# Kernel tuning notes

Measured on AMD Instinct MI355X. Metric: run time of the kernel, lower is better.

## Reference

```python
import jax, jax.numpy as jnp
import numpy as np

S = 10        # spiking_segment_count
TEMP = 50.0

def setup_inputs() -> dict:
    key = jax.random.key(0)
    ks = jax.random.split(key, 6)
    bs, din, dout = 2048, 1024, 1024
    x = jax.random.normal(ks[0], (bs, din), dtype=jnp.float32)
    t = jax.random.uniform(ks[1], (bs,), dtype=jnp.float32)  # in [0,1) subset of [-1,1]
    scale = 1.0 / np.sqrt(din)
    param_W = jax.random.normal(ks[2], (din, dout * S * 3), dtype=jnp.float32) * scale
    param_b = jax.random.normal(ks[3], (dout * S * 3,), dtype=jnp.float32) * 0.01
    norm_W = jax.random.normal(ks[4], (din, dout), dtype=jnp.float32) * scale
    norm_b = jax.random.normal(ks[5], (dout,), dtype=jnp.float32) * 0.01
    return {"x": x, "t": t, "param_W": param_W, "param_b": param_b,
            "norm_W": norm_W, "norm_b": norm_b}

def reference(x, t, param_W, param_b, norm_W, norm_b):
    bs = x.shape[0]
    dout = norm_W.shape[1]
    # param GEMM -> (bs, S, dout, 3)
    params = (x @ param_W + param_b).reshape(bs, S, dout, 3)
    weights = jax.nn.softmax(params[..., 0], axis=1)                 # (bs, S, dout)
    keypoints = jnp.concatenate(
        [jnp.zeros_like(weights[:, :1]), jnp.cumsum(weights, axis=1)], axis=1
    ) * 2.0 - 1.0                                                    # (bs, S+1, dout)
    slopes = jnp.tanh(params[..., 1])
    intercepts = params[..., 2]
    tt = t.reshape(-1, 1, 1)                                         # (bs, 1, 1)
    starts = keypoints[:, :S]
    ends = keypoints[:, 1:]
    residual = slopes * tt + intercepts                              # (bs, S, dout)
    validity = ((tt >= starts) & (tt < ends)) | ((tt == 1.0) & (ends == 1.0))
    vf = validity.astype(x.dtype)
    left_margin = jnp.sum((tt - starts) * vf, axis=1)                # (bs, dout)
    right_margin = jnp.sum((ends - tt) * vf, axis=1)
    lw = jax.nn.sigmoid(-TEMP * left_margin)
    rw = jax.nn.sigmoid(-TEMP * right_margin)
    lv = jnp.concatenate([vf[:, :1], vf[:, :-1]], axis=1)
    rv = jnp.concatenate([vf[:, 1:], vf[:, -1:]], axis=1)
    sw = -(lw + rw - 1.0)
    result = (lw * jnp.sum(residual * lv, axis=1)
              + sw * jnp.sum(residual * vf, axis=1)
              + rw * jnp.sum(residual * rv, axis=1))
    # norm == 'constant': subtract segment-wise integral, add norm_net(x)
    integral = jnp.sum(0.5 * slopes * (ends * ends - starts * starts)
                       + intercepts * weights, axis=1) * 0.5
    norm_target = x @ norm_W + norm_b
    return result - integral + norm_target
```

## Files before the change

kernel.cpp:

```cpp
#include <hip/hip_runtime.h>
#include <cstdint>
#include <cstddef>

#define BS    2048
#define DIN   1024
#define DOUT  1024
#define SSEG  10
#define NPAR  30720
#define NPK   20480
#define NCOL2 21504
#define NLG   10240
#define NT_LG 80
#define NT_SM 168
#define MT    16
#define TAU   5e-5f
#define WL_CAP 1048576u

typedef _Float16 half_t;
typedef __attribute__((ext_vector_type(8))) _Float16 half8;
typedef __attribute__((ext_vector_type(4))) _Float16 half4;
typedef __attribute__((ext_vector_type(2))) _Float16 half2v;
typedef __attribute__((ext_vector_type(4))) float   floatx4;

__device__ __forceinline__ void gload16(const void* g, void* l) {
  __builtin_amdgcn_global_load_lds(
      (const __attribute__((address_space(1))) void*)g,
      (__attribute__((address_space(3))) void*)l, 16, 0, 0);
}

__global__ void k_zero(unsigned* c) { if (threadIdx.x == 0) *c = 0; }

__global__ __launch_bounds__(256) void k_prep(const float* __restrict__ x,
                                              half_t* __restrict__ xh,
                                              half_t* __restrict__ xl,
                                              const float* __restrict__ nW,
                                              half_t* __restrict__ wsm,
                                              unsigned* __restrict__ cnt) {
  int bid = blockIdx.x;
  if (bid < 2048) {
    if (bid == 0 && threadIdx.x == 0) *cnt = 0;
    int i = bid * 256 + threadIdx.x;
    floatx4 v = ((const floatx4*)x)[i];
    half4 h, l;
    #pragma unroll
    for (int c = 0; c < 4; c++) { h[c] = (half_t)v[c]; l[c] = (half_t)(v[c] - (float)h[c]); }
    ((half4*)xh)[i] = h;
    ((half4*)xl)[i] = l;
  } else {
    __shared__ float tile[32][33];
    int b2 = bid - 2048;
    int col0 = (b2 & 31) * 32;
    int k0   = (b2 >> 5) * 32;
    int tx = threadIdx.x & 31;
    int ty = threadIdx.x >> 5;
    #pragma unroll
    for (int r = ty; r < 32; r += 8)
      tile[r][tx] = nW[(size_t)(k0 + r) * DOUT + col0 + tx];
    __syncthreads();
    #pragma unroll
    for (int r = ty; r < 32; r += 8)
      wsm[(size_t)(col0 + r + NPK) * DIN + k0 + tx] = (half_t)tile[tx][r];
  }
}

__global__ __launch_bounds__(256) void k_transw(const float* __restrict__ src,
                                                half_t* __restrict__ wsm,
                                                half_t* __restrict__ wh,
                                                half_t* __restrict__ wlo,
                                                float* __restrict__ wlt) {
  __shared__ float tile[32][384];
  int bx = blockIdx.x;
  int k0 = blockIdx.y * 32;
  int tid = threadIdx.x;
  int s  = bx >> 3;
  int d0 = (bx & 7) * 128;
  const float* sb = src + (size_t)k0 * NPAR + bx * 384;
  for (int i = tid; i < 32 * 96; i += 256) {
    int r = i / 96, q = i - r * 96;
    ((floatx4*)&tile[r][0])[q] = ((const floatx4*)(sb + (size_t)r * NPAR))[q];
  }
  __syncthreads();
  int j   = tid & 127;
  int ks  = (tid >> 7) * 16;
  {
    size_t row = (size_t)(s * 1024 + d0 + j) * DIN + k0 + ks;
    #pragma unroll
    for (int m = 0; m < 16; m++) {
      float raw = tile[ks + m][3 * j];
      float v = raw * 32.0f;
      half_t h = (half_t)v;
      wlt[row + m] = raw;
      wh [row + m] = h;
      wlo[row + m] = (half_t)(v - (float)h);
    }
  }
  #pragma unroll
  for (int c = 0; c < 2; c++) {
    size_t row = (size_t)(s * 2048 + 2 * (d0 + j) + c) * DIN + k0 + ks;
    #pragma unroll
    for (int m = 0; m < 16; m++)
      wsm[row + m] = (half_t)tile[ks + m][3 * j + 1 + c];
  }
}

__device__ __forceinline__ void swizzle_mn(int bid, int* mt, int* nt) {
  int x = bid & 7;
  int g = bid >> 3;
  *mt = g & 15;
  *nt = (g >> 4) * 8 + x;
}

__global__ __launch_bounds__(256) void k_gemm_logit(const half_t* __restrict__ Ah,
                                                    const half_t* __restrict__ Al,
                                                    const half_t* __restrict__ Bh,
                                                    const half_t* __restrict__ Bl,
                                                    float* __restrict__ Lg,
                                                    const float* __restrict__ pb) {
  __shared__ __attribute__((aligned(16))) half_t sAh[128 * 32];
  __shared__ __attribute__((aligned(16))) half_t sAl[128 * 32];
  __shared__ __attribute__((aligned(16))) half_t sBh[128 * 32];
  __shared__ __attribute__((aligned(16))) half_t sBl[128 * 32];
  const int K = DIN;
  int mt, nt;
  swizzle_mn(blockIdx.x, &mt, &nt);
  int m0 = mt * 128, n0 = nt * 128;
  int tid = threadIdx.x, w = tid >> 6, L = tid & 63;
  int wm = (w >> 1) * 64, wn = (w & 1) * 64;
  int l15 = L & 15, quad = L >> 4;

  size_t arow = (size_t)(m0 + w * 16 + (L >> 2)) * K + (L & 3) * 8;
  size_t brow = (size_t)(n0 + w * 16 + (L >> 2)) * K + (L & 3) * 8;
  char* lah = (char*)sAh + w * 1024;
  char* lal = (char*)sAl + w * 1024;
  char* lbh = (char*)sBh + w * 1024;
  char* lbl = (char*)sBl + w * 1024;

  floatx4 acc[4][4] = {};

  for (int k0 = 0; k0 < K; k0 += 32) {
    __syncthreads();
    gload16(Ah + arow + k0,          lah);
    gload16(Ah + arow + 64 * K + k0, lah + 4096);
    gload16(Al + arow + k0,          lal);
    gload16(Al + arow + 64 * K + k0, lal + 4096);
    gload16(Bh + brow + k0,          lbh);
    gload16(Bh + brow + 64 * K + k0, lbh + 4096);
    gload16(Bl + brow + k0,          lbl);
    gload16(Bl + brow + 64 * K + k0, lbl + 4096);
    __syncthreads();

    #pragma unroll
    for (int mi = 0; mi < 4; mi++) {
      half8 afh = *(const half8*)((const char*)sAh + (wm + mi * 16 + l15) * 64 + quad * 16);
      half8 afl = *(const half8*)((const char*)sAl + (wm + mi * 16 + l15) * 64 + quad * 16);
      #pragma unroll
      for (int ni = 0; ni < 4; ni++) {
        half8 bfh = *(const half8*)((const char*)sBh + (wn + ni * 16 + l15) * 64 + quad * 16);
        half8 bfl = *(const half8*)((const char*)sBl + (wn + ni * 16 + l15) * 64 + quad * 16);
        floatx4 a = acc[mi][ni];
        a = __builtin_amdgcn_mfma_f32_16x16x32_f16(afh, bfh, a, 0, 0, 0);
        a = __builtin_amdgcn_mfma_f32_16x16x32_f16(afl, bfh, a, 0, 0, 0);
        a = __builtin_amdgcn_mfma_f32_16x16x32_f16(afh, bfl, a, 0, 0, 0);
        acc[mi][ni] = a;
      }
    }
  }

  #pragma unroll
  for (int ni = 0; ni < 4; ni++) {
    int col = n0 + wn + ni * 16 + l15;
    float bias = pb[(col >> 10) * 3072 + (col & 1023) * 3];
    #pragma unroll
    for (int mi = 0; mi < 4; mi++) {
      int row = m0 + wm + mi * 16 + quad * 4;
      floatx4 v = acc[mi][ni];
      #pragma unroll
      for (int r = 0; r < 4; r++)
        Lg[(size_t)(row + r) * NLG + col] = v[r] * 0.03125f + bias;
    }
  }
}

__global__ __launch_bounds__(256) void k_gemm_sm(const half_t* __restrict__ A,
                                                 const half_t* __restrict__ B,
                                                 half_t* __restrict__ P,
                                                 const float* __restrict__ pb,
                                                 const float* __restrict__ nb) {
  __shared__ __attribute__((aligned(16))) half_t As[128 * 32];
  __shared__ __attribute__((aligned(16))) half_t Bs[128 * 32];
  const int K = DIN;
  int mt, nt;
  swizzle_mn(blockIdx.x, &mt, &nt);
  int m0 = mt * 128, n0 = nt * 128;
  int tid = threadIdx.x, w = tid >> 6, L = tid & 63;
  int wm = (w >> 1) * 64, wn = (w & 1) * 64;
  int l15 = L & 15, quad = L >> 4;

  const half_t* ga = A + (size_t)(m0 + w * 16 + (L >> 2)) * K + (L & 3) * 8;
  const half_t* gb = B + (size_t)(n0 + w * 16 + (L >> 2)) * K + (L & 3) * 8;
  char* lA = (char*)As + w * 1024;
  char* lB = (char*)Bs + w * 1024;

  floatx4 acc[4][4] = {};

  for (int k0 = 0; k0 < K; k0 += 32) {
    __syncthreads();
    gload16(ga + k0,          lA);
    gload16(ga + 64 * K + k0, lA + 4096);
    gload16(gb + k0,          lB);
    gload16(gb + 64 * K + k0, lB + 4096);
    __syncthreads();

    half8 af[4], bf[4];
    #pragma unroll
    for (int mi = 0; mi < 4; mi++)
      af[mi] = *(const half8*)((const char*)As + (wm + mi * 16 + l15) * 64 + quad * 16);
    #pragma unroll
    for (int ni = 0; ni < 4; ni++)
      bf[ni] = *(const half8*)((const char*)Bs + (wn + ni * 16 + l15) * 64 + quad * 16);
    #pragma unroll
    for (int mi = 0; mi < 4; mi++)
      #pragma unroll
      for (int ni = 0; ni < 4; ni++)
        acc[mi][ni] = __builtin_amdgcn_mfma_f32_16x16x32_f16(af[mi], bf[ni], acc[mi][ni], 0, 0, 0);
  }

  #pragma unroll
  for (int ni = 0; ni < 4; ni++) {
    int col = n0 + wn + ni * 16 + l15;
    float bias;
    if (col < NPK) {
      int s = col >> 11, rem = col & 2047;
      bias = pb[s * 3072 + 3 * (rem >> 1) + 1 + (rem & 1)];
    } else {
      bias = nb[col - NPK];
    }
    #pragma unroll
    for (int mi = 0; mi < 4; mi++) {
      int row = m0 + wm + mi * 16 + quad * 4;
      floatx4 v = acc[mi][ni];
      #pragma unroll
      for (int r = 0; r < 4; r++)
        P[(size_t)(row + r) * NCOL2 + col] = (half_t)(v[r] + bias);
    }
  }
}

__device__ __forceinline__ float spiking_eval(const float* p, float tt, float* mind) {
  float mx = -1e30f;
  #pragma unroll
  for (int s = 0; s < SSEG; s++) mx = fmaxf(mx, p[3 * s]);
  float ew[10], wsum = 0.0f;
  #pragma unroll
  for (int s = 0; s < SSEG; s++) { ew[s] = __expf(p[3 * s] - mx); wsum += ew[s]; }
  float inv = 1.0f / wsum;

  float kp[11];
  kp[0] = -1.0f;
  float cum = 0.0f, md = 1e30f;
  #pragma unroll
  for (int s = 0; s < SSEG; s++) {
    cum += ew[s] * inv;
    kp[s + 1] = cum * 2.0f - 1.0f;
    md = fminf(md, fabsf(tt - kp[s + 1]));
  }
  *mind = md;

  float vf[10], resid[10];
  float lm = 0.0f, rm = 0.0f, integ = 0.0f;
  #pragma unroll
  for (int s = 0; s < SSEG; s++) {
    float p1 = p[3 * s + 1], p2 = p[3 * s + 2];
    float e2 = __expf(2.0f * fabsf(p1));
    float th = copysignf(1.0f - 2.0f / (e2 + 1.0f), p1);
    resid[s] = th * tt + p2;
    float st = kp[s], en = kp[s + 1];
    bool v = ((tt >= st) && (tt < en)) || ((tt == 1.0f) && (en == 1.0f));
    float vv = v ? 1.0f : 0.0f;
    vf[s] = vv;
    lm += (tt - st) * vv;
    rm += (en - tt) * vv;
    integ += 0.5f * th * (en * en - st * st) + p2 * (ew[s] * inv);
  }
  float resLV = 0.0f, resV = 0.0f, resRV = 0.0f;
  #pragma unroll
  for (int s = 0; s < SSEG; s++) {
    float lv = (s == 0) ? vf[0] : vf[s - 1];
    float rv = (s == 9) ? vf[9] : vf[s + 1];
    resLV += resid[s] * lv;
    resV  += resid[s] * vf[s];
    resRV += resid[s] * rv;
  }
  float lw = 1.0f / (1.0f + __expf(50.0f * lm));
  float rw = 1.0f / (1.0f + __expf(50.0f * rm));
  float swt = 1.0f - lw - rw;
  return lw * resLV + swt * resV + rw * resRV - 0.5f * integ + p[30];
}

__global__ __launch_bounds__(256) void k_pointwise(const half_t* __restrict__ P,
                                                   const float* __restrict__ Lg,
                                                   const float* __restrict__ t,
                                                   float* __restrict__ out,
                                                   unsigned* __restrict__ cnt,
                                                   unsigned* __restrict__ wl,
                                                   unsigned cap) {
  __shared__ __attribute__((aligned(16))) half_t sp[SSEG * 512];
  int b = blockIdx.x, dg = blockIdx.y, tid = threadIdx.x;
  const half_t* Pb = P + (size_t)b * NCOL2;
  for (int i = tid; i < SSEG * 64; i += 256) {
    int s = i >> 6, e = i & 63;
    ((uint4*)sp)[(s << 6) + e] = ((const uint4*)(Pb + s * 2048 + dg * 512))[e];
  }
  float tt = t[b];
  float nt = (float)Pb[NPK + dg * 256 + tid];
  const float* Lb = Lg + (size_t)b * NLG + dg * 256 + tid;
  __syncthreads();

  float p[31];
  #pragma unroll
  for (int s = 0; s < SSEG; s++) {
    p[3 * s] = Lb[s * 1024];
    half2v hv = ((const half2v*)sp)[s * 256 + tid];
    p[3 * s + 1] = (float)hv.x;
    p[3 * s + 2] = (float)hv.y;
  }
  p[30] = nt;
  float mind;
  float r = spiking_eval(p, tt, &mind);
  int d = dg * 256 + tid;
  out[(size_t)b * DOUT + d] = r;
  if (wl != nullptr && mind < TAU) {
    unsigned idx = atomicAdd(cnt, 1u);
    if (idx < cap) wl[idx] = ((unsigned)b << 10) | (unsigned)d;
  }
}

__global__ __launch_bounds__(256) void k_naive(const float* __restrict__ x,
                                               const float* __restrict__ t,
                                               const float* __restrict__ pW,
                                               const float* __restrict__ pb,
                                               const float* __restrict__ nW,
                                               const float* __restrict__ nb,
                                               float* __restrict__ out,
                                               unsigned* __restrict__ cnt,
                                               unsigned* __restrict__ wl,
                                               unsigned cap) {
  __shared__ float xs[DIN];
  int b = blockIdx.x, dg = blockIdx.y, tid = threadIdx.x;
  for (int i = tid; i < DIN; i += 256) xs[i] = x[(size_t)b * DIN + i];
  __syncthreads();
  int d = dg * 256 + tid;
  float acc[31];
  #pragma unroll
  for (int i = 0; i < 31; i++) acc[i] = 0.0f;
  for (int k = 0; k < DIN; k++) {
    float xv = xs[k];
    const float* wr = pW + (size_t)k * NPAR + 3 * d;
    #pragma unroll
    for (int s = 0; s < SSEG; s++) {
      acc[3 * s]     += xv * wr[s * 3072];
      acc[3 * s + 1] += xv * wr[s * 3072 + 1];
      acc[3 * s + 2] += xv * wr[s * 3072 + 2];
    }
    acc[30] += xv * nW[(size_t)k * DOUT + d];
  }
  #pragma unroll
  for (int s = 0; s < SSEG; s++) {
    acc[3 * s]     += pb[s * 3072 + 3 * d];
    acc[3 * s + 1] += pb[s * 3072 + 3 * d + 1];
    acc[3 * s + 2] += pb[s * 3072 + 3 * d + 2];
  }
  acc[30] += nb[d];
  float mind;
  float r = spiking_eval(acc, t[b], &mind);
  out[(size_t)b * DOUT + d] = r;
  if (wl != nullptr && mind < TAU) {
    unsigned idx = atomicAdd(cnt, 1u);
    if (idx < cap) wl[idx] = ((unsigned)b << 10) | (unsigned)d;
  }
}

__global__ __launch_bounds__(256) void k_redo(const float* __restrict__ x,
                                              const float* __restrict__ t,
                                              const float* __restrict__ pW,
                                              const float* __restrict__ pb,
                                              const float* __restrict__ nW,
                                              const float* __restrict__ nb,
                                              const half_t* __restrict__ P,
                                              const float* __restrict__ WLt,
                                              int haveP,
                                              const unsigned* __restrict__ cnt,
                                              const unsigned* __restrict__ wl,
                                              unsigned cap,
                                              float* __restrict__ out) {
  unsigned n = *cnt;
  if (n > cap) n = cap;
  int lane = threadIdx.x & 63;
  unsigned wave = (blockIdx.x * 256 + threadIdx.x) >> 6;
  unsigned nwaves = (gridDim.x * 256) >> 6;

  for (unsigned e = wave; e < n; e += nwaves) {
    unsigned code = wl[e];
    int b = (int)(code >> 10), d = (int)(code & 1023);

    double lg[10], sl[10], ic[10], nt = 0.0;
    #pragma unroll
    for (int s = 0; s < SSEG; s++) { lg[s] = 0.0; sl[s] = 0.0; ic[s] = 0.0; }

    if (haveP) {
      for (int k = lane; k < DIN; k += 64) {
        double xv = (double)x[(size_t)b * DIN + k];
        #pragma unroll
        for (int s = 0; s < SSEG; s++)
          lg[s] += xv * (double)WLt[(size_t)(s * 1024 + d) * DIN + k];
      }
    } else {
      for (int k = lane; k < DIN; k += 64) {
        double xv = (double)x[(size_t)b * DIN + k];
        const float* wr = pW + (size_t)k * NPAR + 3 * d;
        #pragma unroll
        for (int s = 0; s < SSEG; s++) {
          lg[s] += xv * (double)wr[s * 3072];
          sl[s] += xv * (double)wr[s * 3072 + 1];
          ic[s] += xv * (double)wr[s * 3072 + 2];
        }
        nt += xv * (double)nW[(size_t)k * DOUT + d];
      }
    }
    #pragma unroll
    for (int off = 32; off > 0; off >>= 1) {
      #pragma unroll
      for (int s = 0; s < SSEG; s++) lg[s] += __shfl_down(lg[s], off);
      if (!haveP) {
        #pragma unroll
        for (int s = 0; s < SSEG; s++) {
          sl[s] += __shfl_down(sl[s], off);
          ic[s] += __shfl_down(ic[s], off);
        }
        nt += __shfl_down(nt, off);
      }
    }

    if (lane == 0) {
      double slope[10], icpt[10], ntv;
      if (haveP) {
        const half_t* Pr = P + (size_t)b * NCOL2;
        #pragma unroll
        for (int s = 0; s < SSEG; s++) {
          slope[s] = tanh((double)(float)Pr[s * 2048 + 2 * d]);
          icpt[s]  = (double)(float)Pr[s * 2048 + 2 * d + 1];
        }
        ntv = (double)(float)Pr[NPK + d];
      } else {
        #pragma unroll
        for (int s = 0; s < SSEG; s++) {
          slope[s] = tanh(sl[s] + (double)pb[s * 3072 + 3 * d + 1]);
          icpt[s]  = ic[s] + (double)pb[s * 3072 + 3 * d + 2];
        }
        ntv = nt + (double)nb[d];
      }
      #pragma unroll
      for (int s = 0; s < SSEG; s++) lg[s] += (double)pb[s * 3072 + 3 * d];

      double mx = -1e300;
      #pragma unroll
      for (int s = 0; s < SSEG; s++) mx = fmax(mx, lg[s]);
      double ew[10], ws = 0.0;
      #pragma unroll
      for (int s = 0; s < SSEG; s++) { ew[s] = exp(lg[s] - mx); ws += ew[s]; }

      double kp[11];
      kp[0] = -1.0;
      double cum = 0.0;
      #pragma unroll
      for (int s = 0; s < SSEG; s++) { cum += ew[s] / ws; kp[s + 1] = cum * 2.0 - 1.0; }

      double tt = (double)t[b];
      double vf[10], resid[10], lm = 0.0, rm = 0.0, integ = 0.0;
      #pragma unroll
      for (int s = 0; s < SSEG; s++) {
        double st = kp[s], en = kp[s + 1];
        bool v = ((tt >= st) && (tt < en)) || ((tt == 1.0) && (en == 1.0));
        double vv = v ? 1.0 : 0.0;
        vf[s] = vv;
        resid[s] = slope[s] * tt + icpt[s];
        lm += (tt - st) * vv;
        rm += (en - tt) * vv;
        integ += 0.5 * slope[s] * (en * en - st * st) + icpt[s] * (ew[s] / ws);
      }
      double rLV = 0.0, rV = 0.0, rRV = 0.0;
      #pragma unroll
      for (int s = 0; s < SSEG; s++) {
        double lv = (s == 0) ? vf[0] : vf[s - 1];
        double rv = (s == 9) ? vf[9] : vf[s + 1];
        rLV += resid[s] * lv;
        rV  += resid[s] * vf[s];
        rRV += resid[s] * rv;
      }
      double lw = 1.0 / (1.0 + exp(50.0 * lm));
      double rw = 1.0 / (1.0 + exp(50.0 * rm));
      double res = lw * rLV + (1.0 - lw - rw) * rV + rw * rRV - 0.5 * integ + ntv;
      out[(size_t)b * DOUT + d] = (float)res;
    }
  }
}

extern "C" void kernel_launch(void* const* d_in, const int* in_sizes, int n_in,
                              void* d_out, int out_size, void* d_ws, size_t ws_size,
                              hipStream_t stream) {
  const float* x  = (const float*)d_in[0];
  const float* t  = (const float*)d_in[1];
  const float* pW = (const float*)d_in[2];
  const float* pb = (const float*)d_in[3];
  const float* nW = (const float*)d_in[4];
  const float* nb = (const float*)d_in[5];
  float* out = (float*)d_out;

  const size_t o_cnt = 0;
  const size_t o_wl  = 64;
  const size_t o_xh  = o_wl  + (size_t)WL_CAP * 4;
  const size_t o_xl  = o_xh  + (size_t)BS * DIN * 2;
  const size_t o_wsm = o_xl  + (size_t)BS * DIN * 2;
  const size_t o_wh  = o_wsm + (size_t)NCOL2 * DIN * 2;
  const size_t o_wlo = o_wh  + (size_t)NLG * DIN * 2;
  const size_t o_wlt = o_wlo + (size_t)NLG * DIN * 2;
  const size_t o_p   = o_wlt + (size_t)NLG * DIN * 4;
  const size_t o_lg  = o_p   + (size_t)BS * NCOL2 * 2;
  const size_t need  = o_lg  + (size_t)BS * NLG * 4;

  bool have_wl = ws_size >= 1024 * 1024;
  unsigned* cnt = (unsigned*)((char*)d_ws + o_cnt);
  unsigned* wl  = (unsigned*)((char*)d_ws + o_wl);
  unsigned cap  = 0;
  if (have_wl) {
    size_t avail = (ws_size >= need) ? (size_t)WL_CAP
                                     : (ws_size - o_wl) / 4;
    cap = (unsigned)(avail < WL_CAP ? avail : WL_CAP);
  }

  if (ws_size >= need) {
    half_t* xh  = (half_t*)((char*)d_ws + o_xh);
    half_t* xl  = (half_t*)((char*)d_ws + o_xl);
    half_t* wsm = (half_t*)((char*)d_ws + o_wsm);
    half_t* wh  = (half_t*)((char*)d_ws + o_wh);
    half_t* wlo = (half_t*)((char*)d_ws + o_wlo);
    float*  wlt = (float*)((char*)d_ws + o_wlt);
    half_t* P   = (half_t*)((char*)d_ws + o_p);
    float*  Lg  = (float*)((char*)d_ws + o_lg);

    k_prep<<<3072, 256, 0, stream>>>(x, xh, xl, nW, wsm, cnt);
    k_transw<<<dim3(NPAR / 384, DIN / 32), 256, 0, stream>>>(pW, wsm, wh, wlo, wlt);
    k_gemm_logit<<<NT_LG * MT, 256, 0, stream>>>(xh, xl, wh, wlo, Lg, pb);
    k_gemm_sm<<<NT_SM * MT, 256, 0, stream>>>(xh, wsm, P, pb, nb);
    k_pointwise<<<dim3(BS, DOUT / 256), 256, 0, stream>>>(P, Lg, t, out, cnt,
                                                          have_wl ? wl : nullptr, cap);
    if (have_wl)
      k_redo<<<256, 256, 0, stream>>>(x, t, pW, pb, nW, nb, P, wlt, 1, cnt, wl, cap, out);
  } else {
    if (have_wl) k_zero<<<1, 64, 0, stream>>>(cnt);
    k_naive<<<dim3(BS, DOUT / 256), 256, 0, stream>>>(x, t, pW, pb, nW, nb, out, cnt,
                                                      have_wl ? wl : nullptr, cap);
    if (have_wl)
      k_redo<<<256, 256, 0, stream>>>(x, t, pW, pb, nW, nb, nullptr, nullptr, 0,
                                      cnt, wl, cap, out);
  }
}
```

Baseline: 618.2 us.

## Merge weight transpose into prep kernel with vectorized stores, drop GEMM tile swizzle

Folds the separate parameter-weight transpose kernel into the prep kernel as a third block range, saving one launch and letting the conversion work overlap. The transpose stores are reorganized so each thread writes 16-byte vectors (half8 / float4) of contiguous K elements instead of scalar per-element stores, for better write coalescing. The GEMM kernels switch from a swizzled 1D grid mapping to a plain 2D grid, which may change L2 reuse across tiles. The merged kernel now reserves the large 48KB tile in shared memory for all blocks, which can lower occupancy for the lightweight split blocks.

```diff
diff --git a/kernel.cpp b/kernel.cpp
--- a/kernel.cpp
+++ b/kernel.cpp
@@ -16,6 +16,10 @@
 #define TAU   5e-5f
 #define WL_CAP 1048576u
 
+#define NB_SPLIT 2048
+#define NB_NORM  1024
+#define NB_TRW   2560
+
 typedef _Float16 half_t;
 typedef __attribute__((ext_vector_type(8))) _Float16 half8;
 typedef __attribute__((ext_vector_type(4))) _Float16 half4;
@@ -34,80 +38,94 @@
                                               half_t* __restrict__ xh,
                                               half_t* __restrict__ xl,
                                               const float* __restrict__ nW,
+                                              const float* __restrict__ pW,
                                               half_t* __restrict__ wsm,
+                                              half_t* __restrict__ wh,
+                                              half_t* __restrict__ wlo,
+                                              float* __restrict__ wlt,
                                               unsigned* __restrict__ cnt) {
+  __shared__ float tile[32][384];
   int bid = blockIdx.x;
-  if (bid < 2048) {
-    if (bid == 0 && threadIdx.x == 0) *cnt = 0;
-    int i = bid * 256 + threadIdx.x;
+  int tid = threadIdx.x;
+
+  if (bid < NB_SPLIT) {
+    if (bid == 0 && tid == 0) *cnt = 0;
+    int i = bid * 256 + tid;
     floatx4 v = ((const floatx4*)x)[i];
     half4 h, l;
     #pragma unroll
     for (int c = 0; c < 4; c++) { h[c] = (half_t)v[c]; l[c] = (half_t)(v[c] - (float)h[c]); }
     ((half4*)xh)[i] = h;
     ((half4*)xl)[i] = l;
-  } else {
-    __shared__ float tile[32][33];
-    int b2 = bid - 2048;
+    return;
+  }
+
+  if (bid < NB_SPLIT + NB_NORM) {
+    int b2 = bid - NB_SPLIT;
     int col0 = (b2 & 31) * 32;
     int k0   = (b2 >> 5) * 32;
-    int tx = threadIdx.x & 31;
-    int ty = threadIdx.x >> 5;
+    int tx = tid & 31;
+    int ty = tid >> 5;
+    float* t33 = &tile[0][0];
     #pragma unroll
     for (int r = ty; r < 32; r += 8)
-      tile[r][tx] = nW[(size_t)(k0 + r) * DOUT + col0 + tx];
+      t33[r * 33 + tx] = nW[(size_t)(k0 + r) * DOUT + col0 + tx];
     __syncthreads();
     #pragma unroll
     for (int r = ty; r < 32; r += 8)
-      wsm[(size_t)(col0 + r + NPK) * DIN + k0 + tx] = (half_t)tile[tx][r];
-  }
-}
-
-__global__ __launch_bounds__(256) void k_transw(const float* __restrict__ src,
-                                                half_t* __restrict__ wsm,
-                                                half_t* __restrict__ wh,
-                                                half_t* __restrict__ wlo,
-                                                float* __restrict__ wlt) {
-  __shared__ float tile[32][384];
-  int bx = blockIdx.x;
-  int k0 = blockIdx.y * 32;
-  int tid = threadIdx.x;
+      wsm[(size_t)(col0 + r + NPK) * DIN + k0 + tx] = (half_t)t33[tx * 33 + r];
+    return;
+  }
+
+  int b3 = bid - NB_SPLIT - NB_NORM;
+  int bx = b3 % 80;
+  int k0 = (b3 / 80) * 32;
   int s  = bx >> 3;
   int d0 = (bx & 7) * 128;
-  const float* sb = src + (size_t)k0 * NPAR + bx * 384;
+
+  const float* sb = pW + (size_t)k0 * NPAR + bx * 384;
   for (int i = tid; i < 32 * 96; i += 256) {
     int r = i / 96, q = i - r * 96;
     ((floatx4*)&tile[r][0])[q] = ((const floatx4*)(sb + (size_t)r * NPAR))[q];
   }
   __syncthreads();
-  int j   = tid & 127;
-  int ks  = (tid >> 7) * 16;
-  {
-    size_t row = (size_t)(s * 1024 + d0 + j) * DIN + k0 + ks;
-    #pragma unroll
-    for (int m = 0; m < 16; m++) {
-      float raw = tile[ks + m][3 * j];
-      float v = raw * 32.0f;
-      half_t h = (half_t)v;
-      wlt[row + m] = raw;
-      wh [row + m] = h;
-      wlo[row + m] = (half_t)(v - (float)h);
-    }
-  }
-  #pragma unroll
-  for (int c = 0; c < 2; c++) {
-    size_t row = (size_t)(s * 2048 + 2 * (d0 + j) + c) * DIN + k0 + ks;
-    #pragma unroll
-    for (int m = 0; m < 16; m++)
-      wsm[row + m] = (half_t)tile[ks + m][3 * j + 1 + c];
-  }
-}
-
-__device__ __forceinline__ void swizzle_mn(int bid, int* mt, int* nt) {
-  int x = bid & 7;
-  int g = bid >> 3;
-  *mt = g & 15;
-  *nt = (g >> 4) * 8 + x;
+
+  for (int ci = tid; ci < 3072; ci += 256) {
+    if (ci < 1024) {
+      int rl = ci >> 2, kc = ci & 3;
+      int jj = rl >> 1, cbit = rl & 1;
+      int col = 3 * jj + 1 + cbit;
+      half8 v;
+      #pragma unroll
+      for (int m = 0; m < 8; m++) v[m] = (half_t)tile[kc * 8 + m][col];
+      *(half8*)(wsm + (size_t)(s * 2048 + 2 * (d0 + jj) + cbit) * DIN + k0 + kc * 8) = v;
+    } else if (ci < 1536) {
+      int u = ci - 1024;
+      int jj = u >> 2, kc = u & 3;
+      half8 v;
+      #pragma unroll
+      for (int m = 0; m < 8; m++) v[m] = (half_t)(tile[kc * 8 + m][3 * jj] * 32.0f);
+      *(half8*)(wh + (size_t)(s * 1024 + d0 + jj) * DIN + k0 + kc * 8) = v;
+    } else if (ci < 2048) {
+      int u = ci - 1536;
+      int jj = u >> 2, kc = u & 3;
+      half8 v;
+      #pragma unroll
+      for (int m = 0; m < 8; m++) {
+        float raw = tile[kc * 8 + m][3 * jj] * 32.0f;
+        half_t h = (half_t)raw;
+        v[m] = (half_t)(raw - (float)h);
+      }
+      *(half8*)(wlo + (size_t)(s * 1024 + d0 + jj) * DIN + k0 + kc * 8) = v;
+    } else {
+      int u = ci - 2048;
+      int jj = u >> 3, kc = u & 7;
+      floatx4 v;
+      #pragma unroll
+      for (int m = 0; m < 4; m++) v[m] = tile[kc * 4 + m][3 * jj];
+      *(floatx4*)(wlt + (size_t)(s * 1024 + d0 + jj) * DIN + k0 + kc * 4) = v;
+    }
+  }
 }
 
 __global__ __launch_bounds__(256) void k_gemm_logit(const half_t* __restrict__ Ah,
@@ -121,9 +139,7 @@
   __shared__ __attribute__((aligned(16))) half_t sBh[128 * 32];
   __shared__ __attribute__((aligned(16))) half_t sBl[128 * 32];
   const int K = DIN;
-  int mt, nt;
-  swizzle_mn(blockIdx.x, &mt, &nt);
-  int m0 = mt * 128, n0 = nt * 128;
+  int m0 = blockIdx.y * 128, n0 = blockIdx.x * 128;
   int tid = threadIdx.x, w = tid >> 6, L = tid & 63;
   int wm = (w >> 1) * 64, wn = (w & 1) * 64;
   int l15 = L & 15, quad = L >> 4;
@@ -189,9 +205,7 @@
   __shared__ __attribute__((aligned(16))) half_t As[128 * 32];
   __shared__ __attribute__((aligned(16))) half_t Bs[128 * 32];
   const int K = DIN;
-  int mt, nt;
-  swizzle_mn(blockIdx.x, &mt, &nt);
-  int m0 = mt * 128, n0 = nt * 128;
+  int m0 = blockIdx.y * 128, n0 = blockIdx.x * 128;
   int tid = threadIdx.x, w = tid >> 6, L = tid & 63;
   int wm = (w >> 1) * 64, wn = (w & 1) * 64;
   int l15 = L & 15, quad = L >> 4;
@@ -548,10 +562,10 @@
     half_t* P   = (half_t*)((char*)d_ws + o_p);
     float*  Lg  = (float*)((char*)d_ws + o_lg);
 
-    k_prep<<<3072, 256, 0, stream>>>(x, xh, xl, nW, wsm, cnt);
-    k_transw<<<dim3(NPAR / 384, DIN / 32), 256, 0, stream>>>(pW, wsm, wh, wlo, wlt);
-    k_gemm_logit<<<NT_LG * MT, 256, 0, stream>>>(xh, xl, wh, wlo, Lg, pb);
-    k_gemm_sm<<<NT_SM * MT, 256, 0, stream>>>(xh, wsm, P, pb, nb);
+    k_prep<<<NB_SPLIT + NB_NORM + NB_TRW, 256, 0, stream>>>(x, xh, xl, nW, pW,
+                                                            wsm, wh, wlo, wlt, cnt);
+    k_gemm_logit<<<dim3(NT_LG, MT), 256, 0, stream>>>(xh, xl, wh, wlo, Lg, pb);
+    k_gemm_sm<<<dim3(NT_SM, MT), 256, 0, stream>>>(xh, wsm, P, pb, nb);
     k_pointwise<<<dim3(BS, DOUT / 256), 256, 0, stream>>>(P, Lg, t, out, cnt,
                                                           have_wl ? wl : nullptr, cap);
     if (have_wl)
```

Result: faster. 575.6 us (-6.9%).
